# Optimization experiments

Measured on AMD Instinct MI355X. Metric: run time of the kernel, lower is better.

The kernel has to match this reference:

```python
import jax, jax.numpy as jnp
import numpy as np

M_GROUPS = 1024   # m
N_CELLS = 8       # n, cells per group
K_GROUPS = 128    # k winning groups
K_CELLS = 1       # k_winner_cells per group
GAMMA = 0.5
EPS = 0.5
PRED_GAIN = 1.0
D_IN = 2048
D_OUT = 2048
BSZ = 256


def topk_mask(x, k):
    """Binary mask of top-k entries along last axis. x: [R, D]."""
    _, idx = jax.lax.top_k(x, k)                      # [R, k]
    rows = jnp.arange(x.shape[0])[:, None]
    return jnp.zeros_like(x).at[rows, idx].set(1.0)


def setup_inputs() -> dict:
    key = jax.random.key(0)
    ks = jax.random.split(key, 8)
    total = M_GROUPS * N_CELLS
    return {
        "x_a": jax.random.normal(ks[0], (BSZ, D_IN), jnp.float32),
        "x_b": jax.random.uniform(ks[1], (BSZ, total), jnp.float32),
        "phi": jax.random.uniform(ks[2], (BSZ, total), jnp.float32),
        "psi": jax.random.uniform(ks[3], (BSZ, total), jnp.float32),
        "Wa": jax.random.normal(ks[4], (D_IN, M_GROUPS), jnp.float32) / np.sqrt(D_IN),
        "ba": jnp.zeros((M_GROUPS,), jnp.float32),
        "Wb": jax.random.normal(ks[5], (total, total), jnp.float32) / np.sqrt(total),
        "bb": jnp.zeros((total,), jnp.float32),
        "Wd": jax.random.normal(ks[6], (M_GROUPS, D_OUT), jnp.float32) / np.sqrt(M_GROUPS),
        "bd": jnp.zeros((D_OUT,), jnp.float32),
    }


def reference(x_a, x_b, phi, psi, Wa, ba, Wb, bb, Wd, bd):
    bsz = x_a.shape[0]
    m, n = M_GROUPS, N_CELLS
    total = m * n

    # sigma = repeat_interleave(linear_a(x_a), n) + linear_b(x_b)
    z_a = jnp.repeat(x_a @ Wa + ba, n, axis=1)        # [bsz, total]
    z_b = x_b @ Wb + bb                               # [bsz, total]
    sigma = z_a + z_b

    # inhibited, shifted-positive pi (detached in original)
    pi = jax.lax.stop_gradient((1.0 - phi) * (sigma - sigma.min() + 1.0))

    # per-group top-1 cell mask
    m_pi = topk_mask(pi.reshape(bsz * m, n), K_CELLS).reshape(bsz, total)
    # group max -> top-k group mask, broadcast back to cells
    lambda_ = pi.reshape(bsz, m, n).max(axis=2)       # [bsz, m]
    m_lambda = jnp.repeat(topk_mask(lambda_, K_GROUPS), n, axis=1)

    y = jnp.tanh(m_pi * m_lambda * sigma)             # [bsz, total]

    # decode from group max of y (decode_from_full_memory=False)
    decode_in = y.reshape(bsz, m, n).max(axis=2)      # [bsz, m]
    pred_output = decode_in @ Wd + bd                 # [bsz, d_out]

    phi_new = jnp.maximum(phi * GAMMA, y)
    psi_new = jnp.maximum(psi * EPS, y)
    x_b_new = PRED_GAIN * psi_new                     # x_b_norm=False
    return pred_output, x_b_new, phi_new, psi_new
```

## Files before the change

### kernel.cpp

```cpp
#include <hip/hip_runtime.h>
#include <hip/hip_bf16.h>
#include <cmath>

#define BSZ      256
#define D_IN     2048
#define D_OUT    2048
#define MG       1024
#define NC       8
#define TOTAL    8192
#define KGRP     128

typedef short bf16x8 __attribute__((ext_vector_type(8)));
typedef short s16x4  __attribute__((ext_vector_type(4)));
typedef float f32x4  __attribute__((ext_vector_type(4)));

__device__ inline short f2bf(float f) {
    unsigned u = __float_as_uint(f);
    unsigned r = (u + 0x7fffu + ((u >> 16) & 1u)) >> 16;
    return (short)r;
}
__device__ inline float bf2f(short s) {
    return __uint_as_float(((unsigned)(unsigned short)s) << 16);
}

#define TILE 64
#define BK   32

template <int MODE>
__global__ __launch_bounds__(256) void gemm_f32(
    const float* __restrict__ A, const float* __restrict__ B,
    const float* __restrict__ bias, const float* __restrict__ aux,
    float* __restrict__ C, int M, int N, int K)
{
    __shared__ float As[BK][TILE + 4];
    __shared__ float Bs[BK][TILE];

    const int tid = threadIdx.x;
    const int tx = tid & 15;
    const int ty = tid >> 4;
    const int n0 = blockIdx.x * TILE;
    const int m0 = blockIdx.y * TILE;

    float acc[4][4] = {};

    for (int k0 = 0; k0 < K; k0 += BK) {
        #pragma unroll
        for (int it = 0; it < 2; ++it) {
            int lin = tid + it * 256;
            int row = lin >> 3;
            int c4  = lin & 7;
            float4 a = *(const float4*)&A[(size_t)(m0 + row) * K + k0 + c4 * 4];
            As[c4 * 4 + 0][row] = a.x;
            As[c4 * 4 + 1][row] = a.y;
            As[c4 * 4 + 2][row] = a.z;
            As[c4 * 4 + 3][row] = a.w;
        }
        #pragma unroll
        for (int it = 0; it < 2; ++it) {
            int lin = tid + it * 256;
            int row = lin >> 4;
            int c4  = lin & 15;
            *(float4*)&Bs[row][c4 * 4] =
                *(const float4*)&B[(size_t)(k0 + row) * N + n0 + c4 * 4];
        }
        __syncthreads();

        #pragma unroll
        for (int k = 0; k < BK; ++k) {
            float4 av = *(const float4*)&As[k][ty * 4];
            float4 bv = *(const float4*)&Bs[k][tx * 4];
            float a_[4] = {av.x, av.y, av.z, av.w};
            float b_[4] = {bv.x, bv.y, bv.z, bv.w};
            #pragma unroll
            for (int i = 0; i < 4; ++i)
                #pragma unroll
                for (int j = 0; j < 4; ++j)
                    acc[i][j] = fmaf(a_[i], b_[j], acc[i][j]);
        }
        __syncthreads();
    }

    #pragma unroll
    for (int i = 0; i < 4; ++i) {
        int m = m0 + ty * 4 + i;
        int n = n0 + tx * 4;
        float4 out;
        float* o = (float*)&out;
        #pragma unroll
        for (int j = 0; j < 4; ++j) {
            float v = acc[i][j] + bias[n + j];
            if (MODE == 1) v = aux[(size_t)m * MG + ((n + j) >> 3)] + v;
            o[j] = v;
        }
        *(float4*)&C[(size_t)m * N + n] = out;
    }
}

template <int KSP>
__global__ __launch_bounds__(256) void gemm_f32_ks(
    const float* __restrict__ A, const float* __restrict__ B,
    float* __restrict__ C, int M, int N, int K)
{
    __shared__ float As[BK][TILE + 4];
    __shared__ float Bs[BK][TILE];

    const int tid = threadIdx.x;
    const int tx = tid & 15;
    const int ty = tid >> 4;
    const int n0 = blockIdx.x * TILE;
    const int m0 = blockIdx.y * TILE;
    const int kbeg = blockIdx.z * KSP;

    float acc[4][4] = {};

    for (int k0 = kbeg; k0 < kbeg + KSP; k0 += BK) {
        #pragma unroll
        for (int it = 0; it < 2; ++it) {
            int lin = tid + it * 256;
            int row = lin >> 3;
            int c4  = lin & 7;
            float4 a = *(const float4*)&A[(size_t)(m0 + row) * K + k0 + c4 * 4];
            As[c4 * 4 + 0][row] = a.x;
            As[c4 * 4 + 1][row] = a.y;
            As[c4 * 4 + 2][row] = a.z;
            As[c4 * 4 + 3][row] = a.w;
        }
        #pragma unroll
        for (int it = 0; it < 2; ++it) {
            int lin = tid + it * 256;
            int row = lin >> 4;
            int c4  = lin & 15;
            *(float4*)&Bs[row][c4 * 4] =
                *(const float4*)&B[(size_t)(k0 + row) * N + n0 + c4 * 4];
        }
        __syncthreads();

        #pragma unroll
        for (int k = 0; k < BK; ++k) {
            float4 av = *(const float4*)&As[k][ty * 4];
            float4 bv = *(const float4*)&Bs[k][tx * 4];
            float a_[4] = {av.x, av.y, av.z, av.w};
            float b_[4] = {bv.x, bv.y, bv.z, bv.w};
            #pragma unroll
            for (int i = 0; i < 4; ++i)
                #pragma unroll
                for (int j = 0; j < 4; ++j)
                    acc[i][j] = fmaf(a_[i], b_[j], acc[i][j]);
        }
        __syncthreads();
    }

    float* Cz = C + (size_t)blockIdx.z * M * N;
    #pragma unroll
    for (int i = 0; i < 4; ++i) {
        int m = m0 + ty * 4 + i;
        int n = n0 + tx * 4;
        float4 out;
        float* o = (float*)&out;
        #pragma unroll
        for (int j = 0; j < 4; ++j) o[j] = acc[i][j];
        *(float4*)&Cz[(size_t)m * N + n] = out;
    }
}

__global__ __launch_bounds__(256) void block_min(
    const float* __restrict__ x, int n, float* __restrict__ out)
{
    __shared__ float red[256];
    float v = 3.402823466e+38f;
    for (int i = blockIdx.x * 256 + threadIdx.x; i < n; i += gridDim.x * 256)
        v = fminf(v, x[i]);
    red[threadIdx.x] = v;
    __syncthreads();
    for (int s = 128; s > 0; s >>= 1) {
        if (threadIdx.x < s)
            red[threadIdx.x] = fminf(red[threadIdx.x], red[threadIdx.x + s]);
        __syncthreads();
    }
    if (threadIdx.x == 0) out[blockIdx.x] = red[0];
}

__global__ __launch_bounds__(512) void row_kernel(
    const float* __restrict__ sigma, const float* __restrict__ phi,
    const float* __restrict__ psi, const float* __restrict__ minval,
    float* __restrict__ decode, float* __restrict__ xb_new,
    float* __restrict__ phi_new, float* __restrict__ psi_new)
{
    __shared__ int acell[MG];
    __shared__ int win[MG];
    __shared__ int wsum[8];
    __shared__ int csum[16];

    const int b = blockIdx.x;
    const int tid = threadIdx.x;
    const int lane = tid & 63;
    const int wid = tid >> 6;
    const float smin = minval[0];
    const float* srow = sigma + (size_t)b * TOTAL;
    const float* prow = phi + (size_t)b * TOTAL;
    const float* qrow = psi + (size_t)b * TOTAL;

    unsigned u0 = 0, u1 = 0;
    #pragma unroll
    for (int slot = 0; slot < 2; ++slot) {
        int g = tid + slot * 512;
        float best = -3.402823466e+38f;
        int bc = 0;
        #pragma unroll
        for (int c = 0; c < NC; ++c) {
            float s = srow[g * NC + c];
            float p = prow[g * NC + c];
            float pi = (1.0f - p) * ((s - smin) + 1.0f);
            if (pi > best) { best = pi; bc = c; }
        }
        unsigned bits = __float_as_uint(best);
        unsigned u = (bits & 0x80000000u) ? ~bits : (bits | 0x80000000u);
        if (slot == 0) u0 = u; else u1 = u;
        acell[g] = bc;
    }

    unsigned V = 0;
    #pragma unroll 1
    for (int bit = 31; bit >= 0; --bit) {
        unsigned cand = V | (1u << bit);
        int c = (int)(u0 >= cand) + (int)(u1 >= cand);
        #pragma unroll
        for (int off = 32; off > 0; off >>= 1) c += __shfl_down(c, off);
        if (lane == 0) wsum[wid] = c;
        __syncthreads();
        int tot = wsum[0] + wsum[1] + wsum[2] + wsum[3]
                + wsum[4] + wsum[5] + wsum[6] + wsum[7];
        __syncthreads();
        if (tot >= KGRP) V = cand;
    }
    {
        int c = (int)(u0 > V) + (int)(u1 > V);
        #pragma unroll
        for (int off = 32; off > 0; off >>= 1) c += __shfl_down(c, off);
        if (lane == 0) wsum[wid] = c;
        __syncthreads();
    }
    int nAbove = wsum[0] + wsum[1] + wsum[2] + wsum[3]
               + wsum[4] + wsum[5] + wsum[6] + wsum[7];
    int need = KGRP - nAbove;

    unsigned long long m0 = __ballot(u0 == V);
    unsigned long long m1 = __ballot(u1 == V);
    if (lane == 0) {
        csum[wid]     = __popcll(m0);
        csum[8 + wid] = __popcll(m1);
    }
    __syncthreads();
    unsigned long long below = (lane == 0) ? 0ull : ((~0ull) >> (64 - lane));
    {
        int pre0 = 0;
        for (int c = 0; c < 8; ++c) if (c < wid) pre0 += csum[c];
        int rank0 = pre0 + (int)__popcll(m0 & below);
        int pre1 = 0;
        for (int c = 0; c < 16; ++c) if (c < 8 + wid) pre1 += csum[c];
        int rank1 = pre1 + (int)__popcll(m1 & below);
        win[tid]       = (u0 > V) || (u0 == V && rank0 < need);
        win[tid + 512] = (u1 > V) || (u1 == V && rank1 < need);
    }
    __syncthreads();

    for (int j = tid; j < TOTAL; j += 512) {
        int g = j >> 3, c = j & 7;
        float s = srow[j];
        float y = 0.0f;
        if (win[g] && acell[g] == c) y = tanhf(s);
        float pn = fmaxf(prow[j] * 0.5f, y);
        float qn = fmaxf(qrow[j] * 0.5f, y);
        phi_new[(size_t)b * TOTAL + j] = pn;
        psi_new[(size_t)b * TOTAL + j] = qn;
        xb_new[(size_t)b * TOTAL + j] = qn;
    }

    for (int g = tid; g < MG; g += 512) {
        float d = 0.0f;
        if (win[g]) d = fmaxf(0.0f, tanhf(srow[g * NC + acell[g]]));
        decode[(size_t)b * MG + g] = d;
    }
}

template <int KD>
__global__ __launch_bounds__(256) void convert_bf(
    const float* __restrict__ src, short* __restrict__ h, short* __restrict__ l,
    int nchunks)
{
    for (int t = blockIdx.x * 256 + threadIdx.x; t < nchunks; t += gridDim.x * 256) {
        int row = t / (KD / 8);
        int kc8 = t - row * (KD / 8);
        size_t sidx = (size_t)row * KD + (size_t)kc8 * 8;
        float4 v0 = *(const float4*)&src[sidx];
        float4 v1 = *(const float4*)&src[sidx + 4];
        float vv[8] = {v0.x, v0.y, v0.z, v0.w, v1.x, v1.y, v1.z, v1.w};
        bf16x8 hv, lv;
        #pragma unroll
        for (int e = 0; e < 8; ++e) {
            short hh = f2bf(vv[e]);
            hv[e] = hh;
            lv[e] = f2bf(vv[e] - bf2f(hh));
        }
        size_t dst = ((size_t)((row >> 4) * (KD / 32) + (kc8 >> 2))) * 512
                   + (size_t)(((kc8 & 3) * 16 + (row & 15)) * 8);
        *(bf16x8*)&h[dst] = hv;
        *(bf16x8*)&l[dst] = lv;
    }
}

template <int KD, int BSTRIDE, int KPER, int SPLITZ, int SLICE>
__global__ __launch_bounds__(1024, 1) void gemm_mfma(
    const short* __restrict__ Ah_g, const short* __restrict__ Al_g,
    const float* __restrict__ Bg, float* __restrict__ part_w,
    float* __restrict__ part_d)
{
    __shared__ short Bh[2][256 * 64];
    __shared__ short Bl[2][256 * 64];

    const int tid = threadIdx.x;
    const int l = tid & 63;
    const int w = tid >> 6;
    const int wr = w >> 2;
    const int wc = w & 3;
    const int z  = blockIdx.x;
    const int n0 = blockIdx.y * 256;
    const int k0 = z * KPER;
    constexpr int NSTEP = KPER / 64;

    const int khalf = tid & 1;
    const int kc    = (tid >> 1) & 7;
    const int n4    = (tid >> 4) * 4;

    f32x4 acc[4][4] = {};
    float4 f[4];

    #pragma unroll
    for (int it = 0; it < 4; ++it)
        f[it] = *(const float4*)&Bg[(size_t)(k0 + kc * 8 + khalf * 4 + it) * BSTRIDE + n0 + n4];
    #pragma unroll
    for (int j = 0; j < 4; ++j) {
        s16x4 hv, lv;
        #pragma unroll
        for (int it = 0; it < 4; ++it) {
            float v = ((const float*)&f[it])[j];
            short hh = f2bf(v);
            hv[it] = hh;
            lv[it] = f2bf(v - bf2f(hh));
        }
        int n = n4 + j;
        int off = n * 64 + ((kc ^ (n & 7)) * 8) + khalf * 4;
        *(s16x4*)&Bh[0][off] = hv;
        *(s16x4*)&Bl[0][off] = lv;
    }
    if (NSTEP > 1) {
        #pragma unroll
        for (int it = 0; it < 4; ++it)
            f[it] = *(const float4*)&Bg[(size_t)(k0 + 64 + kc * 8 + khalf * 4 + it) * BSTRIDE + n0 + n4];
    }

    for (int st = 0; st < NSTEP; ++st) {
        const int cur = st & 1;
        const int kw = k0 + st * 64;

        asm volatile("s_waitcnt lgkmcnt(0)" ::: "memory");
        __builtin_amdgcn_sched_barrier(0);
        __builtin_amdgcn_s_barrier();
        __builtin_amdgcn_sched_barrier(0);

        if (st + 1 < NSTEP) {
            #pragma unroll
            for (int j = 0; j < 4; ++j) {
                s16x4 hv, lv;
                #pragma unroll
                for (int it = 0; it < 4; ++it) {
                    float v = ((const float*)&f[it])[j];
                    short hh = f2bf(v);
                    hv[it] = hh;
                    lv[it] = f2bf(v - bf2f(hh));
                }
                int n = n4 + j;
                int off = n * 64 + ((kc ^ (n & 7)) * 8) + khalf * 4;
                *(s16x4*)&Bh[cur ^ 1][off] = hv;
                *(s16x4*)&Bl[cur ^ 1][off] = lv;
            }
        }
        if (st + 2 < NSTEP) {
            const int kn = kw + 128;
            #pragma unroll
            for (int it = 0; it < 4; ++it)
                f[it] = *(const float4*)&Bg[(size_t)(kn + kc * 8 + khalf * 4 + it) * BSTRIDE + n0 + n4];
        }

        #pragma unroll
        for (int kk = 0; kk < 2; ++kk) {
            bf16x8 ah[4], al[4];
            #pragma unroll
            for (int mt = 0; mt < 4; ++mt) {
                size_t base = ((size_t)((wr * 4 + mt) * (KD / 32) + (kw >> 5) + kk)) * 512
                            + (size_t)l * 8;
                ah[mt] = *(const bf16x8*)&Ah_g[base];
                al[mt] = *(const bf16x8*)&Al_g[base];
            }
            const int chunk = kk * 4 + (l >> 4);
            #pragma unroll
            for (int nt = 0; nt < 4; ++nt) {
                int n = wc * 64 + nt * 16 + (l & 15);
                int off = n * 64 + ((chunk ^ (n & 7)) * 8);
                bf16x8 bh = *(const bf16x8*)&Bh[cur][off];
                bf16x8 bl = *(const bf16x8*)&Bl[cur][off];
                #pragma unroll
                for (int mt = 0; mt < 4; ++mt) {
                    acc[mt][nt] = __builtin_amdgcn_mfma_f32_16x16x32_bf16(
                        ah[mt], bh, acc[mt][nt], 0, 0, 0);
                    acc[mt][nt] = __builtin_amdgcn_mfma_f32_16x16x32_bf16(
                        ah[mt], bl, acc[mt][nt], 0, 0, 0);
                    acc[mt][nt] = __builtin_amdgcn_mfma_f32_16x16x32_bf16(
                        al[mt], bh, acc[mt][nt], 0, 0, 0);
                }
            }
        }
    }

    float* P = (z < SPLITZ) ? (part_w + (size_t)z * SLICE)
                            : (part_d + (size_t)(z - SPLITZ) * SLICE);
    #pragma unroll
    for (int mt = 0; mt < 4; ++mt) {
        int m = wr * 64 + mt * 16 + (l >> 4) * 4;
        #pragma unroll
        for (int nt = 0; nt < 4; ++nt) {
            int n = n0 + wc * 64 + nt * 16 + (l & 15);
            #pragma unroll
            for (int r = 0; r < 4; ++r)
                P[(size_t)(m + r) * BSTRIDE + n] = acc[mt][nt][r];
        }
    }
}

template <int NSLW, int NSLD, int NDIM, int MODE, int STR4>
__global__ __launch_bounds__(256) void reduce_part(
    const float* pw, const float* pd, const float* __restrict__ aux,
    const float* __restrict__ bias, float* out,
    float* __restrict__ bmin)
{
    __shared__ float red[256];
    int i = blockIdx.x * 256 + threadIdx.x;
    size_t b4 = (size_t)i * 4;
    float4 s = {0.f, 0.f, 0.f, 0.f};
    #pragma unroll
    for (int sl = 0; sl < NSLW; ++sl) {
        float4 p = *(const float4*)&pw[(size_t)sl * STR4 * 4 + b4];
        s.x += p.x; s.y += p.y; s.z += p.z; s.w += p.w;
    }
    #pragma unroll
    for (int sl = 0; sl < NSLD; ++sl) {
        float4 p = *(const float4*)&pd[(size_t)sl * STR4 * 4 + b4];
        s.x += p.x; s.y += p.y; s.z += p.z; s.w += p.w;
    }
    int col = (int)(b4 & (NDIM - 1));
    float4 bv = *(const float4*)&bias[col];
    float az = 0.f;
    if (MODE == 1) {
        int m = (int)(b4 >> 13);
        az = aux[m * MG + (col >> 3)];
    }
    s.x += bv.x + az; s.y += bv.y + az; s.z += bv.z + az; s.w += bv.w + az;
    *(float4*)&out[b4] = s;

    if (MODE == 1) {
        float v = fminf(fminf(s.x, s.y), fminf(s.z, s.w));
        red[threadIdx.x] = v;
        __syncthreads();
        for (int st = 128; st > 0; st >>= 1) {
            if (threadIdx.x < st)
                red[threadIdx.x] = fminf(red[threadIdx.x], red[threadIdx.x + st]);
            __syncthreads();
        }
        if (threadIdx.x == 0) bmin[blockIdx.x] = red[0];
    }
}

extern "C" void kernel_launch(void* const* d_in, const int* in_sizes, int n_in,
                              void* d_out, int out_size, void* d_ws, size_t ws_size,
                              hipStream_t stream)
{
    const float* x_a = (const float*)d_in[0];
    const float* x_b = (const float*)d_in[1];
    const float* phi = (const float*)d_in[2];
    const float* psi = (const float*)d_in[3];
    const float* Wa  = (const float*)d_in[4];
    const float* ba  = (const float*)d_in[5];
    const float* Wb  = (const float*)d_in[6];
    const float* bb  = (const float*)d_in[7];
    const float* Wd  = (const float*)d_in[8];
    const float* bd  = (const float*)d_in[9];

    float* out = (float*)d_out;
    float* pred    = out;
    float* xb_new  = out + BSZ * D_OUT;
    float* phi_new = out + BSZ * D_OUT + BSZ * TOTAL;
    float* psi_new = out + BSZ * D_OUT + 2 * BSZ * TOTAL;

    float* ws = (float*)d_ws;
    dim3 blk(256);
    dim3 blk512(512);
    dim3 blk1024(1024);

    const size_t OFF_ZA     = 0;
    const size_t OFF_DECODE = 262144;
    const size_t OFF_BMIN   = 524288;
    const size_t OFF_MINV   = 526336;
    const size_t OFF_XBH    = 526352;
    const size_t OFF_XBL    = 1574928;
    const size_t OFF_PART   = 2623504;
    const size_t NEED = (OFF_PART + 10485760) * 4;

    if (ws_size >= NEED) {
        float* z_a    = ws + OFF_ZA;
        float* decode = ws + OFF_DECODE;
        float* bmin   = ws + OFF_BMIN;
        float* minv   = ws + OFF_MINV;
        short* xbh    = (short*)(ws + OFF_XBH);
        short* xbl    = (short*)(ws + OFF_XBL);
        short* dech   = xbh;
        short* decl   = xbl;
        float* part_w = ws + OFF_PART;
        float* part_d = out + BSZ * D_OUT;
        float* sigma  = part_w;

        gemm_f32_ks<512><<<dim3(MG / TILE, BSZ / TILE, 4), blk, 0, stream>>>(
            x_a, Wa, part_w, BSZ, MG, D_IN);
        reduce_part<4, 0, MG, 0, 65536><<<256, blk, 0, stream>>>(
            part_w, part_w, nullptr, ba, z_a, nullptr);

        convert_bf<TOTAL><<<1024, blk, 0, stream>>>(x_b, xbh, xbl, BSZ * TOTAL / 8);
        gemm_mfma<TOTAL, TOTAL, 1024, 5, BSZ * TOTAL>
            <<<dim3(8, 32), blk1024, 0, stream>>>(
                xbh, xbl, Wb, part_w, part_d);
        reduce_part<5, 3, TOTAL, 1, 524288><<<2048, blk, 0, stream>>>(
            part_w, part_d, z_a, bb, sigma, bmin);
        block_min<<<1, blk, 0, stream>>>(bmin, 2048, minv);

        row_kernel<<<BSZ, blk512, 0, stream>>>(
            sigma, phi, psi, minv, decode, xb_new, phi_new, psi_new);

        convert_bf<MG><<<128, blk, 0, stream>>>(decode, dech, decl, BSZ * MG / 8);
        gemm_mfma<MG, D_OUT, 64, 16, BSZ * D_OUT>
            <<<dim3(16, 8), blk1024, 0, stream>>>(
                dech, decl, Wd, part_w, part_w);
        reduce_part<16, 0, D_OUT, 2, 131072><<<512, blk, 0, stream>>>(
            part_w, part_w, nullptr, bd, pred, nullptr);
    } else {
        float* z_a    = ws;
        float* sigma  = ws + 262144;
        float* decode = ws + 262144 + 2097152;
        float* bmin   = ws + 2621440;
        float* minv   = ws + 2622464;

        gemm_f32<0><<<dim3(MG / TILE, BSZ / TILE), blk, 0, stream>>>(
            x_a, Wa, ba, nullptr, z_a, BSZ, MG, D_IN);
        gemm_f32<1><<<dim3(TOTAL / TILE, BSZ / TILE), blk, 0, stream>>>(
            x_b, Wb, bb, z_a, sigma, BSZ, TOTAL, TOTAL);
        block_min<<<1024, blk, 0, stream>>>(sigma, BSZ * TOTAL, bmin);
        block_min<<<1, blk, 0, stream>>>(bmin, 1024, minv);
        row_kernel<<<BSZ, blk512, 0, stream>>>(
            sigma, phi, psi, minv, decode, xb_new, phi_new, psi_new);
        gemm_f32<0><<<dim3(D_OUT / TILE, BSZ / TILE), blk, 0, stream>>>(
            decode, Wd, bd, nullptr, pred, BSZ, D_OUT, MG);
    }
}
```

Baseline: 256.6 us.

## Interleave LDS staging and global prefetch with MFMA phases in split-K GEMM

Splits each 64-wide K step of the split-K GEMM into eight phases, one per (kk, nt) pair. Each phase issues one slice of next-tile conversion and LDS stores, or one global prefetch load, before its MFMA batch, so memory and conversion work is spread across the compute instead of being front-loaded. The MFMA batches run under s_setprio(1) to favour matrix issue across waves. The cost is two workgroup barriers per phase instead of one per step, which adds synchronisation overhead and may stall waves.

```diff
diff --git a/kernel.cpp b/kernel.cpp
--- a/kernel.cpp
+++ b/kernel.cpp
@@ -334,6 +334,7 @@
 
     f32x4 acc[4][4] = {};
     float4 f[4];
+    bf16x8 ah[4], al[4];
 
     #pragma unroll
     for (int it = 0; it < 4; ++it)
@@ -358,67 +359,74 @@
         for (int it = 0; it < 4; ++it)
             f[it] = *(const float4*)&Bg[(size_t)(k0 + 64 + kc * 8 + khalf * 4 + it) * BSTRIDE + n0 + n4];
     }
+    asm volatile("s_waitcnt lgkmcnt(0)" ::: "memory");
+    __builtin_amdgcn_sched_barrier(0);
+    __builtin_amdgcn_s_barrier();
+    __builtin_amdgcn_sched_barrier(0);
 
     for (int st = 0; st < NSTEP; ++st) {
         const int cur = st & 1;
         const int kw = k0 + st * 64;
 
-        asm volatile("s_waitcnt lgkmcnt(0)" ::: "memory");
-        __builtin_amdgcn_sched_barrier(0);
-        __builtin_amdgcn_s_barrier();
-        __builtin_amdgcn_sched_barrier(0);
-
-        if (st + 1 < NSTEP) {
-            #pragma unroll
-            for (int j = 0; j < 4; ++j) {
-                s16x4 hv, lv;
+        #pragma unroll
+        for (int p = 0; p < 8; ++p) {
+            const int kk = p >> 2;
+            const int nt = p & 3;
+
+            const int chunk = kk * 4 + (l >> 4);
+            const int n = wc * 64 + nt * 16 + (l & 15);
+            const int off = n * 64 + ((chunk ^ (n & 7)) * 8);
+            bf16x8 bh = *(const bf16x8*)&Bh[cur][off];
+            bf16x8 bl = *(const bf16x8*)&Bl[cur][off];
+
+            if (nt == 0) {
                 #pragma unroll
-                for (int it = 0; it < 4; ++it) {
-                    float v = ((const float*)&f[it])[j];
-                    short hh = f2bf(v);
-                    hv[it] = hh;
-                    lv[it] = f2bf(v - bf2f(hh));
+                for (int mt = 0; mt < 4; ++mt) {
+                    size_t base = ((size_t)((wr * 4 + mt) * (KD / 32) + (kw >> 5) + kk)) * 512
+                                + (size_t)l * 8;
+                    ah[mt] = *(const bf16x8*)&Ah_g[base];
+                    al[mt] = *(const bf16x8*)&Al_g[base];
                 }
-                int n = n4 + j;
-                int off = n * 64 + ((kc ^ (n & 7)) * 8) + khalf * 4;
-                *(s16x4*)&Bh[cur ^ 1][off] = hv;
-                *(s16x4*)&Bl[cur ^ 1][off] = lv;
             }
-        }
-        if (st + 2 < NSTEP) {
-            const int kn = kw + 128;
-            #pragma unroll
-            for (int it = 0; it < 4; ++it)
-                f[it] = *(const float4*)&Bg[(size_t)(kn + kc * 8 + khalf * 4 + it) * BSTRIDE + n0 + n4];
-        }
-
-        #pragma unroll
-        for (int kk = 0; kk < 2; ++kk) {
-            bf16x8 ah[4], al[4];
+            if (p < 4) {
+                if (st + 1 < NSTEP) {
+                    s16x4 hv, lv;
+                    #pragma unroll
+                    for (int it = 0; it < 4; ++it) {
+                        float v = ((const float*)&f[it])[p];
+                        short hh = f2bf(v);
+                        hv[it] = hh;
+                        lv[it] = f2bf(v - bf2f(hh));
+                    }
+                    int nn = n4 + p;
+                    int o2 = nn * 64 + ((kc ^ (nn & 7)) * 8) + khalf * 4;
+                    *(s16x4*)&Bh[cur ^ 1][o2] = hv;
+                    *(s16x4*)&Bl[cur ^ 1][o2] = lv;
+                }
+            } else {
+                if (st + 2 < NSTEP) {
+                    const int kn = kw + 128;
+                    f[p - 4] = *(const float4*)&Bg[(size_t)(kn + kc * 8 + khalf * 4 + (p - 4)) * BSTRIDE + n0 + n4];
+                }
+            }
+
+            __builtin_amdgcn_s_barrier();
+            asm volatile("s_waitcnt lgkmcnt(0)" ::: "memory");
+            __builtin_amdgcn_sched_barrier(0);
+
+            __builtin_amdgcn_s_setprio(1);
             #pragma unroll
             for (int mt = 0; mt < 4; ++mt) {
-                size_t base = ((size_t)((wr * 4 + mt) * (KD / 32) + (kw >> 5) + kk)) * 512
-                            + (size_t)l * 8;
-                ah[mt] = *(const bf16x8*)&Ah_g[base];
-                al[mt] = *(const bf16x8*)&Al_g[base];
+                acc[mt][nt] = __builtin_amdgcn_mfma_f32_16x16x32_bf16(
+                    ah[mt], bh, acc[mt][nt], 0, 0, 0);
+                acc[mt][nt] = __builtin_amdgcn_mfma_f32_16x16x32_bf16(
+                    ah[mt], bl, acc[mt][nt], 0, 0, 0);
+                acc[mt][nt] = __builtin_amdgcn_mfma_f32_16x16x32_bf16(
+                    al[mt], bh, acc[mt][nt], 0, 0, 0);
             }
-            const int chunk = kk * 4 + (l >> 4);
-            #pragma unroll
-            for (int nt = 0; nt < 4; ++nt) {
-                int n = wc * 64 + nt * 16 + (l & 15);
-                int off = n * 64 + ((chunk ^ (n & 7)) * 8);
-                bf16x8 bh = *(const bf16x8*)&Bh[cur][off];
-                bf16x8 bl = *(const bf16x8*)&Bl[cur][off];
-                #pragma unroll
-                for (int mt = 0; mt < 4; ++mt) {
-                    acc[mt][nt] = __builtin_amdgcn_mfma_f32_16x16x32_bf16(
-                        ah[mt], bh, acc[mt][nt], 0, 0, 0);
-                    acc[mt][nt] = __builtin_amdgcn_mfma_f32_16x16x32_bf16(
-                        ah[mt], bl, acc[mt][nt], 0, 0, 0);
-                    acc[mt][nt] = __builtin_amdgcn_mfma_f32_16x16x32_bf16(
-                        al[mt], bh, acc[mt][nt], 0, 0, 0);
-                }
-            }
+            __builtin_amdgcn_s_setprio(0);
+
+            __builtin_amdgcn_s_barrier();
         }
     }
 
```

Measured after the change: 343.0 us. +33.7%, slower.
